# Performance work log

Measured on AMD Instinct MI355X. Metric: run time of the kernel, lower is better.

The kernel has to match this reference:

```python
import jax, jax.numpy as jnp
import numpy as np

B, N, F, C, L = 8, 1024, 256, 256, 4


def setup_inputs() -> dict:
    key = jax.random.key(0)
    k1, k2, k3 = jax.random.split(key, 3)
    V = jax.random.normal(k1, (B, N, F), dtype=jnp.float32)
    A = jax.random.uniform(k2, (B, N, N, L), dtype=jnp.float32)
    # learned relational weights: (L+1, C, F); index 0 corresponds to the identity (self) edge
    h_weights = jax.random.normal(k3, (L + 1, C, F), dtype=jnp.float32) * 0.05
    return {"V": V, "A": A, "h_weights": h_weights}


def reference(V, A, h_weights):
    # out[b,i,c] = relu( sum_{l,j,f} A_aug[b,i,j,l] * h[l,c,f] * V[b,j,f] )
    # where A_aug = concat(I, A) on the last axis. We avoid materializing the
    # (B, N*C, N*F) intermediate of the naive impl by projecting V first.
    VW = jnp.einsum('bjf,lcf->bljc', V, h_weights)          # (B, L+1, N, C)
    # identity edge (l=0) contributes VW[:,0] directly; remaining L edge types aggregate over A
    out = VW[:, 0] + jnp.einsum('bijl,bljc->bic', A, VW[:, 1:])  # (B, N, C)
    return jax.nn.relu(out)
```

## Files before the change

### kernel.cpp

```cpp
#include <hip/hip_runtime.h>


typedef float          f32x4  __attribute__((ext_vector_type(4)));
typedef __bf16         bf16x8 __attribute__((ext_vector_type(8)));
typedef unsigned short u16x4  __attribute__((ext_vector_type(4)));
typedef unsigned int   u32x4  __attribute__((ext_vector_type(4)));

#define DEV __device__ __forceinline__

DEV void glds16(const void* g, void* l) {
  __builtin_amdgcn_global_load_lds((const __attribute__((address_space(1))) void*)g,
                                   (__attribute__((address_space(3))) void*)l,
                                   16, 0, 0);
}

DEV void cvt8(__bf16* d, f32x4 u, f32x4 v) {
  bf16x8 o;
  o[0]=(__bf16)u[0]; o[1]=(__bf16)u[1]; o[2]=(__bf16)u[2]; o[3]=(__bf16)u[3];
  o[4]=(__bf16)v[0]; o[5]=(__bf16)v[1]; o[6]=(__bf16)v[2]; o[7]=(__bf16)v[3];
  *(bf16x8*)d = o;
}

DEV bf16x8 cvt8r(f32x4 u, f32x4 v) {
  bf16x8 o;
  o[0]=(__bf16)u[0]; o[1]=(__bf16)u[1]; o[2]=(__bf16)u[2]; o[3]=(__bf16)u[3];
  o[4]=(__bf16)v[0]; o[5]=(__bf16)v[1]; o[6]=(__bf16)v[2]; o[7]=(__bf16)v[3];
  return o;
}

DEV unsigned short bfbits(float x) {
  return __builtin_bit_cast(unsigned short, (__bf16)x);
}

__global__ __launch_bounds__(512, 2)
void k1_vw(const float* __restrict__ Vg, const float* __restrict__ Hg,
           unsigned short* __restrict__ W2t, float* __restrict__ VW0)
{
  __shared__ __attribute__((aligned(16))) __bf16 Vs[2][128*64];
  __shared__ __attribute__((aligned(16))) __bf16 Hs[2][320*64];

  const int tid  = threadIdx.x;
  const int lane = tid & 63;
  const int wid  = tid >> 6;
  const int wj   = wid >> 1;
  const int wc   = wid & 1;
  const int li   = lane & 15;
  const int lg   = lane >> 4;

  const int p    = blockIdx.x;
  const int b    = p & 7;
  const int rest = p >> 3;
  const int ct   = rest & 3;
  const int jt   = rest >> 2;
  const int j0   = jt * 128;
  const int c0   = ct * 64;

  const float* sptr[7];
  int sdst[7];
#pragma unroll
  for (int r = 0; r < 2; ++r) {
    int n = r*512 + tid, row = n >> 3, q = n & 7;
    sptr[r] = Vg + (size_t)(b*1024 + j0 + row)*256 + q*8;
    sdst[r] = row*64 + ((q ^ (row & 7))*8);
  }
#pragma unroll
  for (int r = 0; r < 5; ++r) {
    int n = r*512 + tid, row = n >> 3, q = n & 7;
    int l = row >> 6, cl = row & 63;
    sptr[2+r] = Hg + (size_t)(l*256 + c0 + cl)*256 + q*8;
    sdst[2+r] = row*64 + ((q ^ (row & 7))*8);
  }

  f32x4 acc[5][2][2];
#pragma unroll
  for (int l=0;l<5;l++)
#pragma unroll
    for (int x=0;x<2;x++)
#pragma unroll
      for (int y=0;y<2;y++) acc[l][x][y] = (f32x4){0.f,0.f,0.f,0.f};

  {
    f32x4 sa[14];
#pragma unroll
    for (int i=0;i<7;i++) { sa[2*i] = *(const f32x4*)(sptr[i]); sa[2*i+1] = *(const f32x4*)(sptr[i]+4); }
#pragma unroll
    for (int i=0;i<7;i++) {
      __bf16* d = (i < 2) ? &Vs[0][sdst[i]] : &Hs[0][sdst[i]];
      cvt8(d, sa[2*i], sa[2*i+1]);
    }
  }
  __syncthreads();

  int cur = 0;
#pragma unroll 1
  for (int t = 0; t < 4; ++t) {
    const int nxt = cur ^ 1;
    f32x4 sa[14];
    if (t < 3) {
      const int ko = (t+1)*64;
#pragma unroll
      for (int i=0;i<7;i++) { sa[2*i] = *(const f32x4*)(sptr[i]+ko); sa[2*i+1] = *(const f32x4*)(sptr[i]+ko+4); }
    }
    const __bf16* Vsc = &Vs[cur][0];
    const __bf16* Hsc = &Hs[cur][0];
#pragma unroll
    for (int ks = 0; ks < 2; ++ks) {
      bf16x8 hf[10], vf[2];
#pragma unroll
      for (int l=0;l<5;l++)
#pragma unroll
        for (int cm=0;cm<2;cm++) {
          int row = l*64 + wc*32 + cm*16 + li;
          int ch  = (ks*4 + lg) ^ (row & 7);
          hf[l*2+cm] = *(const bf16x8*)(Hsc + row*64 + ch*8);
        }
#pragma unroll
      for (int jn=0;jn<2;jn++) {
        int row = wj*32 + jn*16 + li;
        int ch  = (ks*4 + lg) ^ (row & 7);
        vf[jn] = *(const bf16x8*)(Vsc + row*64 + ch*8);
      }
#pragma unroll
      for (int l=0;l<5;l++)
#pragma unroll
        for (int cm=0;cm<2;cm++)
#pragma unroll
          for (int jn=0;jn<2;jn++)
            acc[l][cm][jn] = __builtin_amdgcn_mfma_f32_16x16x32_bf16(
                hf[l*2+cm], vf[jn], acc[l][cm][jn], 0, 0, 0);
    }
    if (t < 3) {
#pragma unroll
      for (int i=0;i<7;i++) {
        __bf16* d = (i < 2) ? &Vs[nxt][sdst[i]] : &Hs[nxt][sdst[i]];
        cvt8(d, sa[2*i], sa[2*i+1]);
      }
    }
    __syncthreads();
    cur = nxt;
  }

#pragma unroll
  for (int cm=0;cm<2;cm++)
#pragma unroll
    for (int r=0;r<4;r++) {
      const int c = c0 + wc*32 + cm*16 + lg*4 + r;
#pragma unroll
      for (int jn=0;jn<2;jn++) {
        const int j = j0 + wj*32 + jn*16 + li;
        u16x4 pk;
        pk[0] = bfbits(acc[1][cm][jn][r]);
        pk[1] = bfbits(acc[2][cm][jn][r]);
        pk[2] = bfbits(acc[3][cm][jn][r]);
        pk[3] = bfbits(acc[4][cm][jn][r]);
        *(u16x4*)(W2t + (size_t)(b*256 + c)*4096 + (size_t)j*4) = pk;
        VW0[(size_t)(b*1024 + j)*256 + c] = acc[0][cm][jn][r];
      }
    }
}

#define K2_FENCE() do {                                          \
    asm volatile("s_waitcnt lgkmcnt(0)" ::: "memory");           \
    __builtin_amdgcn_sched_barrier(0);                           \
    __builtin_amdgcn_s_barrier();                                \
    __builtin_amdgcn_sched_barrier(0);                           \
  } while (0)

__global__ __launch_bounds__(512, 2)
void k2_gemm(const float* __restrict__ Ag, const unsigned short* __restrict__ W2t,
             unsigned short* __restrict__ part)
{
  __shared__ __attribute__((aligned(16))) __bf16 As[2][128*64];
  __shared__ __attribute__((aligned(16))) __bf16 Bs[2][256*64];

  const int tid  = threadIdx.x;
  const int lane = tid & 63;
  const int wid  = tid >> 6;
  const int wi   = wid >> 2;
  const int wc   = wid & 3;
  const int li   = lane & 15;
  const int lg   = lane >> 4;
  const int ls   = li & 7;

  const int p    = blockIdx.x;
  const int b    = p & 7;
  const int rest = p >> 3;
  const int kt   = rest & 3;
  const int it   = rest >> 2;

  const int i0 = it*128;
  const int k0 = kt*1024;

  const int ar = tid >> 2, aq = tid & 3, as_ = ar & 7;
  const float* asrc = Ag + (size_t)(b*1024 + i0 + ar)*4096 + k0;
  const int awo0 = ar*64 + ((aq     ^ as_)*8);
  const int awo1 = ar*64 + (((aq+4) ^ as_)*8);
  const int ago0 = aq*8;
  const int ago1 = aq*8 + 32;

  const int br = tid >> 1, h = tid & 1, bs_ = br & 7;
  const unsigned short* bsrc = W2t + (size_t)(b*256 + br)*4096 + k0;
  int bwo[4], bgo[4];
#pragma unroll
  for (int j=0;j<4;j++) {
    bwo[j] = br*64 + (((4*h+j) ^ bs_)*8);
    bgo[j] = (4*h+j)*8;
  }

  f32x4 acc[4][4];
#pragma unroll
  for (int m=0;m<4;m++)
#pragma unroll
    for (int n=0;n<4;n++) acc[m][n] = (f32x4){0.f,0.f,0.f,0.f};

  f32x4 aE0,aE1,aE2,aE3, aO0,aO1,aO2,aO3;
  u32x4 bE0,bE1,bE2,bE3, bO0,bO1,bO2,bO3;

#define K2_LOAD(S, t) do {                                                   \
    const float* _ap = asrc + (t)*64;                                        \
    a##S##0 = *(const f32x4*)(_ap + ago0);                                   \
    a##S##1 = *(const f32x4*)(_ap + ago0 + 4);                               \
    a##S##2 = *(const f32x4*)(_ap + ago1);                                   \
    a##S##3 = *(const f32x4*)(_ap + ago1 + 4);                               \
    const unsigned short* _bp = bsrc + (t)*64;                               \
    b##S##0 = *(const u32x4*)(_bp + bgo[0]);                                 \
    b##S##1 = *(const u32x4*)(_bp + bgo[1]);                                 \
    b##S##2 = *(const u32x4*)(_bp + bgo[2]);                                 \
    b##S##3 = *(const u32x4*)(_bp + bgo[3]);                                 \
  } while (0)

#define K2_DSW(S, X) do {                                                    \
    *(bf16x8*)(&As[X][awo0]) = cvt8r(a##S##0, a##S##1);                      \
    *(bf16x8*)(&As[X][awo1]) = cvt8r(a##S##2, a##S##3);                      \
    *(u32x4*)(&Bs[X][bwo[0]]) = b##S##0;                                     \
    *(u32x4*)(&Bs[X][bwo[1]]) = b##S##1;                                     \
    *(u32x4*)(&Bs[X][bwo[2]]) = b##S##2;                                     \
    *(u32x4*)(&Bs[X][bwo[3]]) = b##S##3;                                     \
  } while (0)

#define K2_COMP(X) do {                                                      \
    _Pragma("unroll")                                                        \
    for (int kk=0;kk<2;kk++) {                                               \
      bf16x8 af[4];                                                          \
      _Pragma("unroll")                                                      \
      for (int m=0;m<4;m++) {                                                \
        int row = wi*64 + m*16 + li;                                         \
        af[m] = *(const bf16x8*)(&As[X][row*64 + (((kk*4+lg) ^ ls)*8)]);     \
      }                                                                      \
      _Pragma("unroll")                                                      \
      for (int np=0;np<2;np++) {                                             \
        bf16x8 bf0, bf1;                                                     \
        {                                                                    \
          int row0 = wc*64 + (np*2  )*16 + li;                               \
          int row1 = wc*64 + (np*2+1)*16 + li;                               \
          bf0 = *(const bf16x8*)(&Bs[X][row0*64 + (((kk*4+lg) ^ ls)*8)]);    \
          bf1 = *(const bf16x8*)(&Bs[X][row1*64 + (((kk*4+lg) ^ ls)*8)]);    \
        }                                                                    \
        __builtin_amdgcn_s_setprio(1);                                       \
        _Pragma("unroll")                                                    \
        for (int m=0;m<4;m++) {                                              \
          acc[m][np*2  ] = __builtin_amdgcn_mfma_f32_16x16x32_bf16(          \
              af[m], bf0, acc[m][np*2  ], 0, 0, 0);                          \
          acc[m][np*2+1] = __builtin_amdgcn_mfma_f32_16x16x32_bf16(          \
              af[m], bf1, acc[m][np*2+1], 0, 0, 0);                          \
        }                                                                    \
        __builtin_amdgcn_s_setprio(0);                                       \
      }                                                                      \
    }                                                                        \
  } while (0)

  K2_LOAD(E, 0);
  K2_LOAD(O, 1);
  K2_DSW(E, 0);
  K2_FENCE();

#pragma unroll 1
  for (int u = 0; u < 7; ++u) {
    K2_LOAD(E, 2*u+2);
    K2_DSW(O, 1);
    K2_COMP(0);
    K2_FENCE();

    K2_LOAD(O, 2*u+3);
    K2_DSW(E, 0);
    K2_COMP(1);
    K2_FENCE();
  }
  K2_DSW(O, 1);
  K2_COMP(0);
  K2_FENCE();
  K2_COMP(1);

#undef K2_LOAD
#undef K2_DSW
#undef K2_COMP

  unsigned short* pb = part + (size_t)kt*2097152u + (size_t)(b*1024 + i0)*256;
#pragma unroll
  for (int m=0;m<4;m++)
#pragma unroll
    for (int r=0;r<4;r++) {
      const int il = wi*64 + m*16 + lg*4 + r;
#pragma unroll
      for (int n=0;n<4;n++) {
        const int cl = wc*64 + n*16 + li;
        pb[(size_t)il*256 + cl] = bfbits(acc[m][n][r]);
      }
    }
}

__global__ __launch_bounds__(256)
void k3_reduce(const unsigned short* __restrict__ part, const float* __restrict__ VW0,
               float* __restrict__ out)
{
  const size_t i8 = ((size_t)blockIdx.x*256 + threadIdx.x)*8;
  f32x4 s0 = *(const f32x4*)(VW0 + i8);
  f32x4 s1 = *(const f32x4*)(VW0 + i8 + 4);
#pragma unroll
  for (int q=0;q<4;q++) {
    u32x4 u = *(const u32x4*)(part + (size_t)q*2097152u + i8);
    s0[0] += __uint_as_float(u[0] << 16);  s0[1] += __uint_as_float(u[0] & 0xffff0000u);
    s0[2] += __uint_as_float(u[1] << 16);  s0[3] += __uint_as_float(u[1] & 0xffff0000u);
    s1[0] += __uint_as_float(u[2] << 16);  s1[1] += __uint_as_float(u[2] & 0xffff0000u);
    s1[2] += __uint_as_float(u[3] << 16);  s1[3] += __uint_as_float(u[3] & 0xffff0000u);
  }
#pragma unroll
  for (int e=0;e<4;e++){ s0[e] = fmaxf(s0[e],0.f); s1[e] = fmaxf(s1[e],0.f); }
  *(f32x4*)(out + i8)     = s0;
  *(f32x4*)(out + i8 + 4) = s1;
}

extern "C" void kernel_launch(void* const* d_in, const int* in_sizes, int n_in,
                              void* d_out, int out_size, void* d_ws, size_t ws_size,
                              hipStream_t stream) {
  const float* Vg = (const float*)d_in[0];
  const float* Ag = (const float*)d_in[1];
  const float* Hg = (const float*)d_in[2];
  float* out = (float*)d_out;

  if (ws_size < 41943040u) return;
  char* ws = (char*)d_ws;
  unsigned short* W2t  = (unsigned short*)(ws);
  float*          VW0  = (float*)(ws + 16777216u);
  unsigned short* part = (unsigned short*)(ws + 16777216u + 8388608u);

  k1_vw    <<<dim3(256),  dim3(512), 0, stream>>>(Vg, Hg, W2t, VW0);
  k2_gemm  <<<dim3(256),  dim3(512), 0, stream>>>(Ag, W2t, part);
  k3_reduce<<<dim3(1024), dim3(256), 0, stream>>>(part, VW0, out);
}
```

Measured before the change: 51.46 us.

## Fuse split-K reduction into GEMM via last-block atomic counter

Removes the separate reduce kernel. Each GEMM block bumps a per-(batch, row-tile) atomic counter after writing its bf16 partial, and the fourth block to arrive sums the four partials with VW0, applies ReLU and writes the output. This saves one kernel launch and lets the reduction overlap with other GEMM blocks. In exchange it adds a memset launch, threadfences, and a serial tail in which one 512-thread block reduces 128x256 elements.

```diff
diff --git a/kernel.cpp b/kernel.cpp
--- a/kernel.cpp
+++ b/kernel.cpp
@@ -7,12 +7,6 @@
 typedef unsigned int   u32x4  __attribute__((ext_vector_type(4)));
 
 #define DEV __device__ __forceinline__
-
-DEV void glds16(const void* g, void* l) {
-  __builtin_amdgcn_global_load_lds((const __attribute__((address_space(1))) void*)g,
-                                   (__attribute__((address_space(3))) void*)l,
-                                   16, 0, 0);
-}
 
 DEV void cvt8(__bf16* d, f32x4 u, f32x4 v) {
   bf16x8 o;
@@ -168,10 +162,12 @@
 
 __global__ __launch_bounds__(512, 2)
 void k2_gemm(const float* __restrict__ Ag, const unsigned short* __restrict__ W2t,
-             unsigned short* __restrict__ part)
+             unsigned short* __restrict__ part, const float* __restrict__ VW0,
+             float* __restrict__ out, int* __restrict__ cnt)
 {
   __shared__ __attribute__((aligned(16))) __bf16 As[2][128*64];
   __shared__ __attribute__((aligned(16))) __bf16 Bs[2][256*64];
+  __shared__ int red_flag;
 
   const int tid  = threadIdx.x;
   const int lane = tid & 63;
@@ -307,27 +303,35 @@
         pb[(size_t)il*256 + cl] = bfbits(acc[m][n][r]);
       }
     }
-}
-
-__global__ __launch_bounds__(256)
-void k3_reduce(const unsigned short* __restrict__ part, const float* __restrict__ VW0,
-               float* __restrict__ out)
-{
-  const size_t i8 = ((size_t)blockIdx.x*256 + threadIdx.x)*8;
-  f32x4 s0 = *(const f32x4*)(VW0 + i8);
-  f32x4 s1 = *(const f32x4*)(VW0 + i8 + 4);
-#pragma unroll
-  for (int q=0;q<4;q++) {
-    u32x4 u = *(const u32x4*)(part + (size_t)q*2097152u + i8);
-    s0[0] += __uint_as_float(u[0] << 16);  s0[1] += __uint_as_float(u[0] & 0xffff0000u);
-    s0[2] += __uint_as_float(u[1] << 16);  s0[3] += __uint_as_float(u[1] & 0xffff0000u);
-    s1[0] += __uint_as_float(u[2] << 16);  s1[1] += __uint_as_float(u[2] & 0xffff0000u);
-    s1[2] += __uint_as_float(u[3] << 16);  s1[3] += __uint_as_float(u[3] & 0xffff0000u);
-  }
-#pragma unroll
-  for (int e=0;e<4;e++){ s0[e] = fmaxf(s0[e],0.f); s1[e] = fmaxf(s1[e],0.f); }
-  *(f32x4*)(out + i8)     = s0;
-  *(f32x4*)(out + i8 + 4) = s1;
+
+  __threadfence();
+  if (tid == 0) {
+    int old = atomicAdd(&cnt[(b<<3) + it], 1);
+    red_flag = (old == 3);
+  }
+  __syncthreads();
+  if (red_flag) {
+    __threadfence();
+    const size_t base = (size_t)(b*1024 + i0)*256;
+#pragma unroll 1
+    for (int r = 0; r < 8; ++r) {
+      const size_t i8 = base + (size_t)(r*512 + tid)*8;
+      f32x4 s0 = *(const f32x4*)(VW0 + i8);
+      f32x4 s1 = *(const f32x4*)(VW0 + i8 + 4);
+#pragma unroll
+      for (int q=0;q<4;q++) {
+        u32x4 u = *(const u32x4*)(part + (size_t)q*2097152u + i8);
+        s0[0] += __uint_as_float(u[0] << 16);  s0[1] += __uint_as_float(u[0] & 0xffff0000u);
+        s0[2] += __uint_as_float(u[1] << 16);  s0[3] += __uint_as_float(u[1] & 0xffff0000u);
+        s1[0] += __uint_as_float(u[2] << 16);  s1[1] += __uint_as_float(u[2] & 0xffff0000u);
+        s1[2] += __uint_as_float(u[3] << 16);  s1[3] += __uint_as_float(u[3] & 0xffff0000u);
+      }
+#pragma unroll
+      for (int e=0;e<4;e++){ s0[e] = fmaxf(s0[e],0.f); s1[e] = fmaxf(s1[e],0.f); }
+      *(f32x4*)(out + i8)     = s0;
+      *(f32x4*)(out + i8 + 4) = s1;
+    }
+  }
 }
 
 extern "C" void kernel_launch(void* const* d_in, const int* in_sizes, int n_in,
@@ -338,13 +342,14 @@
   const float* Hg = (const float*)d_in[2];
   float* out = (float*)d_out;
 
-  if (ws_size < 41943040u) return;
+  if (ws_size < 41944064u) return;
   char* ws = (char*)d_ws;
   unsigned short* W2t  = (unsigned short*)(ws);
   float*          VW0  = (float*)(ws + 16777216u);
   unsigned short* part = (unsigned short*)(ws + 16777216u + 8388608u);
-
-  k1_vw    <<<dim3(256),  dim3(512), 0, stream>>>(Vg, Hg, W2t, VW0);
-  k2_gemm  <<<dim3(256),  dim3(512), 0, stream>>>(Ag, W2t, part);
-  k3_reduce<<<dim3(1024), dim3(256), 0, stream>>>(part, VW0, out);
-}
+  int*            cnt  = (int*)(ws + 41943040u);
+
+  hipMemsetAsync(cnt, 0, 64*sizeof(int), stream);
+  k1_vw  <<<dim3(256), dim3(512), 0, stream>>>(Vg, Hg, W2t, VW0);
+  k2_gemm<<<dim3(256), dim3(512), 0, stream>>>(Ag, W2t, part, VW0, out, cnt);
+}
```

Result: slower. 135.6 us (+163.4%).
